# Performance work log

Hardware: AMD Instinct MI355X
Metric: run time of the kernel (lower is better)

## Reference

```python
import jax, jax.numpy as jnp
import numpy as np

# dims: L layers, T steps, N envs, D d_model, H heads, DH d_head, M mem_len, DI d_inner
L, T, N, D, H, DH, M, DI = 6, 128, 32, 1024, 16, 64, 128, 4096


def _layer_norm(x, g, b, eps=1e-5):
    mu = jnp.mean(x, axis=-1, keepdims=True)
    var = jnp.mean(jnp.square(x - mu), axis=-1, keepdims=True)
    return (x - mu) * jax.lax.rsqrt(var + eps) * g + b


def _rel_shift(x):
    # x: (n, h, q, k) with k axis indexed by relative distance (k-1 .. 0)
    n, h, q, k = x.shape
    x = jnp.pad(x, ((0, 0), (0, 0), (0, 0), (1, 0)))
    x = x.reshape(n, h, k + 1, q)[:, :, 1:, :].reshape(n, h, q, k)
    return x


def setup_inputs() -> dict:
    key = jax.random.key(0)
    ks = jax.random.split(key, 16)
    s = 0.02
    inp = {
        "x": jax.random.normal(ks[0], (T * N, D), jnp.float32),
        "context": jax.random.normal(ks[1], (T * N, D), jnp.float32),
        "mems": jax.random.normal(ks[2], (L, N, M, D), jnp.float32),
        "masks": jnp.ones((T * N,), jnp.float32),
        "Wq": jax.random.normal(ks[3], (L, D, H * DH), jnp.float32) * s,
        "Wk": jax.random.normal(ks[4], (L, D, H * DH), jnp.float32) * s,
        "Wv": jax.random.normal(ks[5], (L, D, H * DH), jnp.float32) * s,
        "Wr": jax.random.normal(ks[6], (L, D, H * DH), jnp.float32) * s,
        "Wo": jax.random.normal(ks[7], (L, H * DH, D), jnp.float32) * s,
        "W1": jax.random.normal(ks[8], (L, D, DI), jnp.float32) * s,
        "b1": jnp.zeros((L, DI), jnp.float32),
        "W2": jax.random.normal(ks[9], (L, DI, D), jnp.float32) * s,
        "b2": jnp.zeros((L, D), jnp.float32),
        "ln1_g": jnp.ones((L, D), jnp.float32),
        "ln1_b": jnp.zeros((L, D), jnp.float32),
        "ln2_g": jnp.ones((L, D), jnp.float32),
        "ln2_b": jnp.zeros((L, D), jnp.float32),
        "r_w_bias": jax.random.normal(ks[10], (H, DH), jnp.float32) * s,
        "r_r_bias": jax.random.normal(ks[11], (H, DH), jnp.float32) * s,
    }
    return inp


def reference(x, context, mems, masks, Wq, Wk, Wv, Wr, Wo, W1, b1, W2, b2,
              ln1_g, ln1_b, ln2_g, ln2_b, r_w_bias, r_r_bias):
    n = mems.shape[1]
    t = x.shape[0] // n
    m = mems.shape[2]
    klen = m + t
    dh = r_w_bias.shape[-1]
    h_heads = r_w_bias.shape[0]

    xs = x.reshape(t, n, -1)
    ctx = context.reshape(t, n, -1)
    mk = masks.reshape(t, n)

    # zero memories for envs that reset at the first step (mems * masks)
    mems = mems * mk[0][None, :, None, None]

    # episode-reset attention mask: token i attends token j iff j<=i and no
    # reset (mask==0) happened between them; memory visible only before any reset
    ep = jnp.cumsum((mk == 0.0).astype(jnp.int32), axis=0)  # (t, n)
    epT = ep.T  # (n, t)
    causal = jnp.tril(jnp.ones((t, t), bool))
    allow_seq = causal[None, :, :] & (epT[:, :, None] == epT[:, None, :])  # (n,t,t)
    allow_mem = jnp.broadcast_to((epT == 0)[:, :, None], (n, t, m))  # (n,t,m)
    allow = jnp.concatenate([allow_mem, allow_seq], axis=-1)[:, None]  # (n,1,t,K)

    # sinusoidal relative position embedding, distances klen-1 .. 0
    pos = jnp.arange(klen - 1, -1, -1, dtype=x.dtype)
    inv_freq = 1.0 / (10000.0 ** (jnp.arange(0, xs.shape[-1], 2, dtype=x.dtype) / xs.shape[-1]))
    ang = pos[:, None] * inv_freq[None, :]
    R = jnp.concatenate([jnp.sin(ang), jnp.cos(ang)], axis=-1)  # (K, D)

    h = xs + ctx  # fuse observation features with goal context
    scale = 1.0 / jnp.sqrt(jnp.asarray(dh, x.dtype))

    n_layer = mems.shape[0]
    for l in range(n_layer):
        cat = jnp.concatenate([jnp.transpose(mems[l], (1, 0, 2)), h], axis=0)  # (K,n,D)
        q = (h @ Wq[l]).reshape(t, n, h_heads, dh)
        k = (cat @ Wk[l]).reshape(klen, n, h_heads, dh)
        v = (cat @ Wv[l]).reshape(klen, n, h_heads, dh)
        r = (R @ Wr[l]).reshape(klen, h_heads, dh)
        AC = jnp.einsum('inhd,jnhd->nhij', q + r_w_bias, k)
        BD = _rel_shift(jnp.einsum('inhd,jhd->nhij', q + r_r_bias, r))
        score = (AC + BD) * scale
        score = jnp.where(allow, score, -1e9)
        attn = jax.nn.softmax(score, axis=-1)
        o = jnp.einsum('nhij,jnhd->inhd', attn, v).reshape(t, n, h_heads * dh) @ Wo[l]
        h = _layer_norm(h + o, ln1_g[l], ln1_b[l])
        f = jax.nn.relu(h @ W1[l] + b1[l]) @ W2[l] + b2[l]
        h = _layer_norm(h + f, ln2_g[l], ln2_b[l])

    return h.reshape(t * n, -1)
```

## Files before the change

kernel.cpp:

```cpp
#include <hip/hip_runtime.h>
#include <stdint.h>

#define DEV static __device__ __forceinline__

typedef __attribute__((ext_vector_type(4))) float f32x4;
typedef __attribute__((ext_vector_type(8))) short bf16x8;
typedef __attribute__((ext_vector_type(4))) short s16x4;

static constexpr int L_ = 6, T_ = 128, NE = 32, D_ = 1024, H_ = 16, DH_ = 64, M_ = 128, DI_ = 4096;
static constexpr int KLEN = M_ + T_;
static constexpr int TN = T_ * NE;
static constexpr int NB = NE * H_;

DEV unsigned short f2bf(float f) {
  unsigned u = __builtin_bit_cast(unsigned, f);
  u += 0x7FFFu + ((u >> 16) & 1u);
  return (unsigned short)(u >> 16);
}
DEV float bf2f(unsigned short h) {
  unsigned u = ((unsigned)h) << 16;
  return __builtin_bit_cast(float, u);
}

DEV void gload16(const unsigned short* g, unsigned short* lds) {
  __builtin_amdgcn_global_load_lds(
      (const __attribute__((address_space(1))) unsigned int*)g,
      (__attribute__((address_space(3))) unsigned int*)lds, 16, 0, 0);
}

#define WAITV0 asm volatile("s_waitcnt vmcnt(0)" ::: "memory")

DEV void stage128(const unsigned short* __restrict__ Ab, int lda,
                  const unsigned short* __restrict__ Bb, int ldb,
                  unsigned short* lA, unsigned short* lB,
                  int m0, int n0, int k0, int w, int l)
{
#pragma unroll
  for (int i = 0; i < 4; ++i) {
    const int obb = i * 4096 + w * 1024;
    const int ob  = obb + (l << 4);
    const int row = ob >> 7;
    const int col = (((ob >> 4) & 7) ^ (row & 7)) << 3;
    gload16(Ab + (size_t)(m0 + row) * lda + k0 + col, lA + (obb >> 1));
    gload16(Bb + (size_t)(n0 + row) * ldb + k0 + col, lB + (obb >> 1));
  }
}

DEV void compute128(const unsigned short* lA, const unsigned short* lB,
                    int w, int l, f32x4 acc[4][4])
{
  const int wr = (w >> 1) * 64, wc = (w & 1) * 64;
  const int lan = l & 15, lgr = l >> 4;
#pragma unroll
  for (int ks = 0; ks < 2; ++ks) {
    bf16x8 av[4], bv[4];
#pragma unroll
    for (int m = 0; m < 4; ++m) {
      const int row = wr + m * 16 + lan;
      const int byte = ((row << 7) + (ks << 6) + (lgr << 4)) ^ ((row & 7) << 4);
      av[m] = *(const bf16x8*)((const char*)lA + byte);
    }
#pragma unroll
    for (int n = 0; n < 4; ++n) {
      const int row = wc + n * 16 + lan;
      const int byte = ((row << 7) + (ks << 6) + (lgr << 4)) ^ ((row & 7) << 4);
      bv[n] = *(const bf16x8*)((const char*)lB + byte);
    }
#pragma unroll
    for (int m = 0; m < 4; ++m)
#pragma unroll
      for (int n = 0; n < 4; ++n)
        acc[m][n] = __builtin_amdgcn_mfma_f32_16x16x32_bf16(av[m], bv[n], acc[m][n], 0, 0, 0);
  }
}

DEV void gemm128_2ph(const unsigned short* __restrict__ Ab, int lda,
                     const unsigned short* __restrict__ Bb, int ldb,
                     unsigned short (*shA)[8192], unsigned short (*shB)[8192],
                     int m0, int n0, int nK, int w, int l, f32x4 acc[4][4])
{
  stage128(Ab, lda, Bb, ldb, shA[0], shB[0], m0, n0, 0, w, l);
  WAITV0;
  __syncthreads();
  int cur = 0;
  for (int kt = 0; kt < nK; ++kt) {
    if (kt + 1 < nK)
      stage128(Ab, lda, Bb, ldb, shA[cur ^ 1], shB[cur ^ 1], m0, n0, (kt + 1) * 64, w, l);
    compute128(shA[cur], shB[cur], w, l, acc);
    WAITV0;
    __syncthreads();
    cur ^= 1;
  }
}

template <int EPI>
__global__ __launch_bounds__(256) void gemm_bt(
    const unsigned short* __restrict__ A, int lda, int sAn, int sAh,
    const unsigned short* __restrict__ B, int ldb, int sBn, int sBh,
    void* __restrict__ Cv, int ldc, int sC,
    const float* __restrict__ bias, int nK, int Hb)
{
  __shared__ unsigned short shA[2][8192];
  __shared__ unsigned short shB[2][8192];

  const int z = blockIdx.z;
  const int bn = z / Hb, bh = z % Hb;
  const unsigned short* Ab = A + (size_t)bn * sAn + (size_t)bh * sAh;
  const unsigned short* Bb = B + (size_t)bn * sBn + (size_t)bh * sBh;
  const int m0 = blockIdx.y * 128;
  const int n0 = blockIdx.x * 128;

  const int t = threadIdx.x;
  const int w = t >> 6, l = t & 63;
  const int wr = (w >> 1) * 64, wc = (w & 1) * 64;
  const int lan = l & 15, lgr = l >> 4;

  f32x4 acc[4][4];
#pragma unroll
  for (int m = 0; m < 4; ++m)
#pragma unroll
    for (int n = 0; n < 4; ++n) acc[m][n] = (f32x4){0.f, 0.f, 0.f, 0.f};

  gemm128_2ph(Ab, lda, Bb, ldb, shA, shB, m0, n0, nK, w, l, acc);

  const int zc = z * sC;
#pragma unroll
  for (int m = 0; m < 4; ++m) {
    const int row = m0 + wr + m * 16 + lgr * 4;
#pragma unroll
    for (int n = 0; n < 4; ++n) {
      const int col = n0 + wc + n * 16 + lan;
      const float bcol = (EPI >= 2) ? bias[col] : 0.f;
#pragma unroll
      for (int e = 0; e < 4; ++e) {
        float v = acc[m][n][e];
        const size_t idx = (size_t)zc + (size_t)(row + e) * ldc + col;
        if (EPI == 0) {
          ((float*)Cv)[idx] = v;
        } else if (EPI == 1) {
          ((unsigned short*)Cv)[idx] = f2bf(v);
        } else if (EPI == 2) {
          v += bcol; v = v > 0.f ? v : 0.f;
          ((unsigned short*)Cv)[idx] = f2bf(v);
        } else {
          ((float*)Cv)[idx] = v + bcol;
        }
      }
    }
  }
}

__global__ __launch_bounds__(256) void gemm_proj(
    const unsigned short* __restrict__ catA, const unsigned short* __restrict__ wt,
    unsigned short* __restrict__ kb, unsigned short* __restrict__ vb,
    unsigned short* __restrict__ qw, unsigned short* __restrict__ qr,
    unsigned short* __restrict__ rb,
    const float* __restrict__ rwb, const float* __restrict__ rrb)
{
  __shared__ unsigned short shA[2][8192];
  __shared__ unsigned short shB[2][8192];

  const int id = blockIdx.x;
  int by, bx;
  if (id < 1024)      { by = id >> 4;               bx = id & 15; }
  else if (id < 1280) { const int u = id - 1024; by = 32 + (u >> 3); bx = 16 + (u & 7); }
  else                { const int u = id - 1280; by = 64 + (u >> 3); bx = 24 + (u & 7); }
  const int m0 = by * 128, n0 = bx * 128;

  const int t = threadIdx.x;
  const int w = t >> 6, l = t & 63;
  const int wr = (w >> 1) * 64, wc = (w & 1) * 64;
  const int lan = l & 15, lgr = l >> 4;

  f32x4 acc[4][4];
#pragma unroll
  for (int m = 0; m < 4; ++m)
#pragma unroll
    for (int n = 0; n < 4; ++n) acc[m][n] = (f32x4){0.f, 0.f, 0.f, 0.f};

  gemm128_2ph(catA, 1024, wt, 1024, shA, shB, m0, n0, 16, w, l, acc);

#pragma unroll
  for (int m = 0; m < 4; ++m) {
    const int row = m0 + wr + m * 16 + lgr * 4;
#pragma unroll
    for (int n = 0; n < 4; ++n) {
      const int col = n0 + wc + n * 16 + lan;
#pragma unroll
      for (int e = 0; e < 4; ++e) {
        const float v = acc[m][n][e];
        const int r = row + e;
        if (col < 1024) {
          kb[(size_t)r * 1024 + col] = f2bf(v);
        } else if (col < 2048) {
          vb[(size_t)r * 1024 + col - 1024] = f2bf(v);
        } else if (col < 3072) {
          const int c = col - 2048;
          const size_t o = (size_t)(r - 4096) * 1024 + c;
          qw[o] = f2bf(v + rwb[c]);
          qr[o] = f2bf(v + rrb[c]);
        } else {
          const int c = col - 3072;
          rb[(size_t)(r - 8192) * 1024 + c] = f2bf(v);
        }
      }
    }
  }
}

__global__ __launch_bounds__(256) void vtrans_kernel(
    const unsigned short* __restrict__ V, unsigned short* __restrict__ vt)
{
  __shared__ unsigned short tile[128][72];
  const int z = blockIdx.x;
  const int nn = z >> 4, hh = z & 15;
  const int t = threadIdx.x;
  for (int p = 0; p < 2; ++p) {
    const int j = p * 128 + (t >> 1);
    const int dbase = (t & 1) * 32;
    const unsigned short* src = &V[(size_t)(j * NE + nn) * 1024 + hh * 64 + dbase];
#pragma unroll
    for (int i = 0; i < 4; ++i)
      *(bf16x8*)&tile[t >> 1][dbase + i * 8] = *(const bf16x8*)&src[i * 8];
    __syncthreads();
    const int d = t >> 2, jseg = (t & 3) * 32;
    unsigned short out[32];
#pragma unroll
    for (int jj = 0; jj < 32; ++jj) out[jj] = tile[jseg + jj][d];
    unsigned short* dst = &vt[((size_t)z * 64 + d) * 256 + p * 128 + jseg];
#pragma unroll
    for (int i = 0; i < 4; ++i)
      *(bf16x8*)&dst[i * 8] = *(const bf16x8*)&out[i * 8];
    __syncthreads();
  }
}

__global__ __launch_bounds__(256) void attn_kernel(
    const unsigned short* __restrict__ qw, const unsigned short* __restrict__ qr,
    const unsigned short* __restrict__ kbf, const unsigned short* __restrict__ rbf,
    const int* __restrict__ ep, const unsigned short* __restrict__ vt,
    unsigned short* __restrict__ O)
{
  __shared__ unsigned short sS[4][32 * 256];

  const int z = blockIdx.x;
  const int nn = z >> 4, hh = z & 15;
  const int t = threadIdx.x, w = t >> 6, l = t & 63;
  const int lan = l & 15, lgr = l >> 4;
  const int i0 = w * 32;
  unsigned short* S = sS[w];

  bf16x8 av[2][2];
#pragma unroll
  for (int m = 0; m < 2; ++m)
#pragma unroll
    for (int kk = 0; kk < 2; ++kk) {
      const int i = i0 + m * 16 + lan;
      av[m][kk] = *(const bf16x8*)&qw[(size_t)(i * NE + nn) * 1024 + hh * 64 + kk * 32 + lgr * 8];
    }
#pragma unroll
  for (int n = 0; n < 16; ++n) {
    bf16x8 bv[2];
#pragma unroll
    for (int kk = 0; kk < 2; ++kk) {
      const int j = n * 16 + lan;
      bv[kk] = *(const bf16x8*)&kbf[(size_t)(j * NE + nn) * 1024 + hh * 64 + kk * 32 + lgr * 8];
    }
#pragma unroll
    for (int m = 0; m < 2; ++m) {
      f32x4 a4 = (f32x4){0.f, 0.f, 0.f, 0.f};
#pragma unroll
      for (int kk = 0; kk < 2; ++kk)
        a4 = __builtin_amdgcn_mfma_f32_16x16x32_bf16(av[m][kk], bv[kk], a4, 0, 0, 0);
#pragma unroll
      for (int e = 0; e < 4; ++e) {
        const int r = m * 16 + lgr * 4 + e;
        const int j = n * 16 + lan;
        const int swz = ((r >> 2) & 3) * 16;
        S[r * 256 + (j ^ swz)] = f2bf(a4[e]);
      }
    }
  }

  bf16x8 bq[2][2];
#pragma unroll
  for (int m = 0; m < 2; ++m)
#pragma unroll
    for (int kk = 0; kk < 2; ++kk) {
      const int i = i0 + m * 16 + lan;
      bq[m][kk] = *(const bf16x8*)&qr[(size_t)(i * NE + nn) * 1024 + hh * 64 + kk * 32 + lgr * 8];
    }
#pragma unroll
  for (int n = 0; n < 16; ++n) {
    bf16x8 bv[2];
#pragma unroll
    for (int kk = 0; kk < 2; ++kk) {
      const int jp = n * 16 + lan;
      bv[kk] = *(const bf16x8*)&rbf[(size_t)jp * 1024 + hh * 64 + kk * 32 + lgr * 8];
    }
#pragma unroll
    for (int m = 0; m < 2; ++m) {
      f32x4 a4 = (f32x4){0.f, 0.f, 0.f, 0.f};
#pragma unroll
      for (int kk = 0; kk < 2; ++kk)
        a4 = __builtin_amdgcn_mfma_f32_16x16x32_bf16(bq[m][kk], bv[kk], a4, 0, 0, 0);
#pragma unroll
      for (int e = 0; e < 4; ++e) {
        const int r = m * 16 + lgr * 4 + e;
        const int i = i0 + r;
        const int jp = n * 16 + lan;
        const int j = jp + i - 127;
        if (j >= 0 && j < 256) {
          const int swz = ((r >> 2) & 3) * 16;
          const int idx = r * 256 + (j ^ swz);
          S[idx] = f2bf(bf2f(S[idx]) + a4[e]);
        }
      }
    }
  }

  const int j0 = l * 4;
  for (int rr = 0; rr < 32; ++rr) {
    const int i = i0 + rr;
    const int epi = ep[i * NE + nn];
    const int swz = ((rr >> 2) & 3) * 16;
    s16x4 s4 = *(const s16x4*)&S[rr * 256 + (j0 ^ swz)];
    float sc[4];
#pragma unroll
    for (int q = 0; q < 4; ++q) {
      const int j = j0 + q;
      bool allow;
      if (j < M_) {
        allow = (epi == 0);
      } else {
        const int jp = j - M_;
        allow = (jp <= i) && (ep[jp * NE + nn] == epi);
      }
      sc[q] = allow ? bf2f((unsigned short)s4[q]) * 0.125f : -1e9f;
    }
    float mx = fmaxf(fmaxf(sc[0], sc[1]), fmaxf(sc[2], sc[3]));
#pragma unroll
    for (int o = 32; o; o >>= 1) mx = fmaxf(mx, __shfl_xor(mx, o));
    float p[4], sum = 0.f;
#pragma unroll
    for (int q = 0; q < 4; ++q) { p[q] = __expf(sc[q] - mx); sum += p[q]; }
#pragma unroll
    for (int o = 32; o; o >>= 1) sum += __shfl_xor(sum, o);
    const float inv = 1.f / sum;
    s16x4 o4;
#pragma unroll
    for (int q = 0; q < 4; ++q) o4[q] = (short)f2bf(p[q] * inv);
    *(s16x4*)&S[rr * 256 + (j0 ^ swz)] = o4;
  }

  const unsigned short* vtz = vt + (size_t)z * 64 * 256;
  f32x4 acc[2][4];
#pragma unroll
  for (int m = 0; m < 2; ++m)
#pragma unroll
    for (int n = 0; n < 4; ++n) acc[m][n] = (f32x4){0.f, 0.f, 0.f, 0.f};

  for (int ks = 0; ks < 8; ++ks) {
    const int kb = ks * 32 + lgr * 8;
    bf16x8 bv2[4];
#pragma unroll
    for (int n = 0; n < 4; ++n) {
      const int d = n * 16 + lan;
      bv2[n] = *(const bf16x8*)&vtz[(size_t)d * 256 + kb];
    }
    bf16x8 pa[2];
#pragma unroll
    for (int m = 0; m < 2; ++m) {
      const int r = m * 16 + lan;
      const int swz = ((r >> 2) & 3) * 16;
      pa[m] = *(const bf16x8*)&S[r * 256 + (kb ^ swz)];
    }
#pragma unroll
    for (int m = 0; m < 2; ++m)
#pragma unroll
      for (int n = 0; n < 4; ++n)
        acc[m][n] = __builtin_amdgcn_mfma_f32_16x16x32_bf16(pa[m], bv2[n], acc[m][n], 0, 0, 0);
  }
#pragma unroll
  for (int m = 0; m < 2; ++m)
#pragma unroll
    for (int n = 0; n < 4; ++n)
#pragma unroll
      for (int e = 0; e < 4; ++e) {
        const int i = i0 + m * 16 + lgr * 4 + e;
        const int d = n * 16 + lan;
        O[(size_t)(i * NE + nn) * 1024 + hh * DH_ + d] = f2bf(acc[m][n][e]);
      }
}

__global__ __launch_bounds__(256) void transpose13_kernel(
    const float* __restrict__ Wk, const float* __restrict__ Wv,
    const float* __restrict__ Wq, const float* __restrict__ Wr,
    const float* __restrict__ Wo, const float* __restrict__ W1,
    const float* __restrict__ W2,
    unsigned short* __restrict__ wtAll, unsigned short* __restrict__ wto,
    unsigned short* __restrict__ wt1, unsigned short* __restrict__ wt2)
{
  __shared__ float tile[32][33];
  const int zz = blockIdx.z;
  const float* W; unsigned short* WT; int Nd, Kd;
  if (zz < 5) {
    W = (zz == 0) ? Wk : (zz == 1) ? Wv : (zz == 2) ? Wq : (zz == 3) ? Wr : Wo;
    WT = (zz == 4) ? wto : (wtAll + (size_t)zz * 1024 * 1024);
    Nd = 1024; Kd = 1024;
  } else if (zz < 9) {
    const int c = zz - 5;
    W = W1 + (size_t)c * 1024;
    WT = wt1 + (size_t)c * 1024 * 1024;
    Nd = 4096; Kd = 1024;
  } else {
    const int c = zz - 9;
    W = W2 + (size_t)c * 1024 * 1024;
    WT = wt2 + (size_t)c * 1024;
    Nd = 1024; Kd = 4096;
  }
  const int tx = threadIdx.x & 31, ty = threadIdx.x >> 5;
  const int nIn = blockIdx.x * 32 + tx;
  const int kBase = blockIdx.y * 32;
#pragma unroll
  for (int r = 0; r < 32; r += 8)
    tile[ty + r][tx] = W[(size_t)(kBase + ty + r) * Nd + nIn];
  __syncthreads();
#pragma unroll
  for (int r = 0; r < 32; r += 8)
    WT[(size_t)(blockIdx.x * 32 + ty + r) * Kd + kBase + tx] = f2bf(tile[tx][ty + r]);
}

__global__ __launch_bounds__(256) void catmem_kernel(
    const float* __restrict__ mems_l, const float* __restrict__ masks,
    unsigned short* __restrict__ cat)
{
  const int idx = blockIdx.x * 256 + threadIdx.x;
  const int d = idx & 1023;
  const int r = idx >> 10;
  const int nn = r & 31, j = r >> 5;
  const float mk0 = masks[nn];
  cat[idx] = f2bf(mems_l[(size_t)(nn * M_ + j) * 1024 + d] * mk0);
}

__global__ __launch_bounds__(256) void hprep_kernel(
    const float* __restrict__ x, const float* __restrict__ ctx,
    float* __restrict__ h, unsigned short* __restrict__ catUp)
{
  const int idx = blockIdx.x * 256 + threadIdx.x;
  const float v = x[idx] + ctx[idx];
  h[idx] = v;
  catUp[idx] = f2bf(v);
}

__global__ __launch_bounds__(256) void rpos_kernel(unsigned short* __restrict__ R)
{
  const int idx = blockIdx.x * 256 + threadIdx.x;
  const int d = idx & 1023, j = idx >> 10;
  const float pos = (float)(KLEN - 1 - j);
  const int f = d & 511;
  const float inv_freq = __expf(-((float)(2 * f) * (1.f / 1024.f)) * 9.210340371976184f);
  const float ang = pos * inv_freq;
  const float v = (d < 512) ? sinf(ang) : cosf(ang);
  R[idx] = f2bf(v);
}

__global__ void ep_kernel(const float* __restrict__ masks, int* __restrict__ ep)
{
  const int nn = threadIdx.x;
  if (nn < NE) {
    int c = 0;
    for (int i = 0; i < T_; ++i) {
      c += (masks[i * NE + nn] == 0.f) ? 1 : 0;
      ep[i * NE + nn] = c;
    }
  }
}

template <int NP>
__global__ __launch_bounds__(256) void ln_kernel(
    const float* __restrict__ a, const float* __restrict__ parts, size_t pstride,
    const float* __restrict__ bias,
    const float* __restrict__ g, const float* __restrict__ bb,
    float* __restrict__ outf, unsigned short* __restrict__ outbf)
{
  const int row = blockIdx.x;
  const int t = threadIdx.x, w = t >> 6, l = t & 63;
  const int c = t * 4;
  const size_t base = (size_t)row * 1024;
  f32x4 v = *(const f32x4*)&a[base + c];
#pragma unroll
  for (int i = 0; i < NP; ++i)
    v = v + *(const f32x4*)&parts[i * pstride + base + c];
  if (bias) v = v + *(const f32x4*)&bias[c];
  float s = v[0] + v[1] + v[2] + v[3];
#pragma unroll
  for (int o = 32; o; o >>= 1) s += __shfl_xor(s, o);
  __shared__ float red[8];
  if (l == 0) red[w] = s;
  __syncthreads();
  s = red[0] + red[1] + red[2] + red[3];
  const float mu = s * (1.f / 1024.f);
  f32x4 dv = v - mu;
  float s2 = dv[0]*dv[0] + dv[1]*dv[1] + dv[2]*dv[2] + dv[3]*dv[3];
#pragma unroll
  for (int o = 32; o; o >>= 1) s2 += __shfl_xor(s2, o);
  if (l == 0) red[4 + w] = s2;
  __syncthreads();
  s2 = red[4] + red[5] + red[6] + red[7];
  const float inv = rsqrtf(s2 * (1.f / 1024.f) + 1e-5f);
  f32x4 y;
#pragma unroll
  for (int q = 0; q < 4; ++q) y[q] = dv[q] * inv * g[c + q] + bb[c + q];
  *(f32x4*)&outf[base + c] = y;
  if (outbf) {
    s16x4 o4;
#pragma unroll
    for (int q = 0; q < 4; ++q) o4[q] = (short)f2bf(y[q]);
    *(s16x4*)&outbf[base + c] = o4;
  }
}

extern "C" void kernel_launch(void* const* d_in, const int* in_sizes, int n_in,
                              void* d_out, int out_size, void* d_ws, size_t ws_size,
                              hipStream_t stream)
{
  (void)in_sizes; (void)n_in; (void)out_size; (void)ws_size;
  const float* x    = (const float*)d_in[0];
  const float* ctx  = (const float*)d_in[1];
  const float* mems = (const float*)d_in[2];
  const float* masks= (const float*)d_in[3];
  const float* Wq   = (const float*)d_in[4];
  const float* Wk   = (const float*)d_in[5];
  const float* Wv   = (const float*)d_in[6];
  const float* Wr   = (const float*)d_in[7];
  const float* Wo   = (const float*)d_in[8];
  const float* W1   = (const float*)d_in[9];
  const float* b1   = (const float*)d_in[10];
  const float* W2   = (const float*)d_in[11];
  const float* b2   = (const float*)d_in[12];
  const float* ln1g = (const float*)d_in[13];
  const float* ln1b = (const float*)d_in[14];
  const float* ln2g = (const float*)d_in[15];
  const float* ln2b = (const float*)d_in[16];
  const float* rwb  = (const float*)d_in[17];
  const float* rrb  = (const float*)d_in[18];

  char* ws = (char*)d_ws;
  size_t off = 0;
  auto alloc = [&](size_t bytes) {
    char* p = ws + off;
    off += (bytes + 255) & ~(size_t)255;
    return p;
  };
  unsigned short* wtAll = (unsigned short*)alloc(4096u * 1024 * 2);
  unsigned short* wto = (unsigned short*)alloc(1024u * 1024 * 2);
  unsigned short* wt1 = (unsigned short*)alloc(4096u * 1024 * 2);
  unsigned short* wt2 = (unsigned short*)alloc(4096u * 1024 * 2);
  unsigned short* cat = (unsigned short*)alloc((size_t)(KLEN * NE + 256) * 1024 * 2);
  unsigned short* rbf = (unsigned short*)alloc((size_t)KLEN * 1024 * 2);
  int*            epb = (int*)alloc((size_t)T_ * NE * 4);
  float*          h   = (float*)alloc((size_t)TN * 1024 * 4);
  float*          h1  = (float*)alloc((size_t)TN * 1024 * 4);
  unsigned short* qw  = (unsigned short*)alloc((size_t)TN * 1024 * 2);
  unsigned short* qr  = (unsigned short*)alloc((size_t)TN * 1024 * 2);
  unsigned short* kbf = (unsigned short*)alloc((size_t)KLEN * NE * 1024 * 2);
  unsigned short* vbf = (unsigned short*)alloc((size_t)KLEN * NE * 1024 * 2);
  unsigned short* vt  = (unsigned short*)alloc((size_t)NB * DH_ * KLEN * 2);
  unsigned short* ACb = (unsigned short*)alloc((size_t)NB * T_ * KLEN * 2);
  unsigned short* BDb = (unsigned short*)alloc((size_t)NB * T_ * KLEN * 2);
  unsigned short* obf = (unsigned short*)alloc((size_t)TN * 1024 * 2);

  unsigned short* catUp = cat + (size_t)M_ * NE * 1024;
  unsigned short* catR  = cat + (size_t)KLEN * NE * 1024;
  unsigned short* f1 = ACb;
  float* part = (float*)BDb;
  unsigned short* h1bf = qw;

  rpos_kernel<<<KLEN * 1024 / 256, 256, 0, stream>>>(catR);
  ep_kernel<<<1, 64, 0, stream>>>(masks, epb);
  hprep_kernel<<<TN * 1024 / 256, 256, 0, stream>>>(x, ctx, h, catUp);

  for (int l = 0; l < L_; ++l) {
    const size_t wOff = (size_t)l * 1024 * 1024;
    const size_t wOffBig = (size_t)l * 1024 * 4096;
    transpose13_kernel<<<dim3(32, 32, 13), 256, 0, stream>>>(
        Wk + wOff, Wv + wOff, Wq + wOff, Wr + wOff, Wo + wOff,
        W1 + wOffBig, W2 + wOffBig, wtAll, wto, wt1, wt2);
    catmem_kernel<<<M_ * NE * 1024 / 256, 256, 0, stream>>>(
        mems + (size_t)l * NE * M_ * 1024, masks, cat);

    gemm_proj<<<1296, 256, 0, stream>>>(cat, wtAll, kbf, vbf, qw, qr, rbf, rwb, rrb);

    vtrans_kernel<<<NB, 256, 0, stream>>>(vbf, vt);

    attn_kernel<<<NB, 256, 0, stream>>>(qw, qr, kbf, rbf, epb, vt, obf);

    gemm_bt<0><<<dim3(8, 32, 2), 256, 0, stream>>>(obf, 1024, 0, 512,
                                                   wto, 1024, 0, 512,
                                                   part, 1024, TN * 1024, nullptr, 8, 2);
    ln_kernel<2><<<TN, 256, 0, stream>>>(h, part, (size_t)TN * 1024, nullptr,
                                         ln1g + l * 1024, ln1b + l * 1024, h1, h1bf);

    gemm_bt<2><<<dim3(32, 32, 1), 256, 0, stream>>>(h1bf, 1024, 0, 0, wt1, 1024, 0, 0,
                                                    f1, 4096, 0, b1 + l * 4096, 16, 1);
    gemm_bt<0><<<dim3(8, 32, 2), 256, 0, stream>>>(f1, 4096, 0, 2048,
                                                   wt2, 4096, 0, 2048,
                                                   part, 1024, TN * 1024, nullptr, 32, 2);
    ln_kernel<2><<<TN, 256, 0, stream>>>(h1, part, (size_t)TN * 1024, b2 + l * 1024,
                                         ln2g + l * 1024, ln2b + l * 1024,
                                         (l == L_ - 1) ? (float*)d_out : h, catUp);
  }
}
```

Baseline: 1.935 ms.

## Remap GEMM blocks for XCD-aware L2 locality and drop V transpose kernel

The GEMM kernels now use a 1D grid and remap block IDs so consecutive blocks on each of the 8 XCDs cover a column strip of 8 tiles. This aims to improve L2 reuse of A and B tiles across the chiplets. Separately, the V transpose kernel is removed, and the attention kernel gathers V directly with strided scalar loads (8 per vector). That saves a launch and a round trip through memory, but the scattered 2-byte loads in the PV loop are uncoalesced and may be slow.

```diff
diff --git a/kernel.cpp b/kernel.cpp
--- a/kernel.cpp
+++ b/kernel.cpp
@@ -98,17 +98,27 @@
     const unsigned short* __restrict__ A, int lda, int sAn, int sAh,
     const unsigned short* __restrict__ B, int ldb, int sBn, int sBh,
     void* __restrict__ Cv, int ldc, int sC,
-    const float* __restrict__ bias, int nK, int Hb)
+    const float* __restrict__ bias, int nK, int Hb, int gx, int gy)
 {
   __shared__ unsigned short shA[2][8192];
   __shared__ unsigned short shB[2][8192];
 
-  const int z = blockIdx.z;
+  const int nwg = gridDim.x;
+  const int bid = blockIdx.x;
+  const int id = (bid & 7) * (nwg >> 3) + (bid >> 3);
+  const int pg = gx * gy;
+  const int z = id / pg;
+  const int rem = id - z * pg;
+  const int sc = rem / (gy * 8);
+  const int within = rem - sc * (gy * 8);
+  const int by = within >> 3;
+  const int bx = sc * 8 + (within & 7);
+
   const int bn = z / Hb, bh = z % Hb;
   const unsigned short* Ab = A + (size_t)bn * sAn + (size_t)bh * sAh;
   const unsigned short* Bb = B + (size_t)bn * sBn + (size_t)bh * sBh;
-  const int m0 = blockIdx.y * 128;
-  const int n0 = blockIdx.x * 128;
+  const int m0 = by * 128;
+  const int n0 = bx * 128;
 
   const int t = threadIdx.x;
   const int w = t >> 6, l = t & 63;
@@ -139,11 +149,9 @@
           ((float*)Cv)[idx] = v;
         } else if (EPI == 1) {
           ((unsigned short*)Cv)[idx] = f2bf(v);
-        } else if (EPI == 2) {
+        } else {
           v += bcol; v = v > 0.f ? v : 0.f;
           ((unsigned short*)Cv)[idx] = f2bf(v);
-        } else {
-          ((float*)Cv)[idx] = v + bcol;
         }
       }
     }
@@ -160,11 +168,21 @@
   __shared__ unsigned short shA[2][8192];
   __shared__ unsigned short shB[2][8192];
 
-  const int id = blockIdx.x;
+  const int bid = blockIdx.x;
+  const int id = (bid & 7) * 162 + (bid >> 3);
   int by, bx;
-  if (id < 1024)      { by = id >> 4;               bx = id & 15; }
-  else if (id < 1280) { const int u = id - 1024; by = 32 + (u >> 3); bx = 16 + (u & 7); }
-  else                { const int u = id - 1280; by = 64 + (u >> 3); bx = 24 + (u & 7); }
+  if (id < 1024) {
+    const int sc = id >> 9;
+    const int within = id & 511;
+    by = within >> 3;
+    bx = sc * 8 + (within & 7);
+  } else if (id < 1280) {
+    const int u = id - 1024;
+    by = 32 + (u >> 3); bx = 16 + (u & 7);
+  } else {
+    const int u = id - 1280;
+    by = 64 + (u >> 3); bx = 24 + (u & 7);
+  }
   const int m0 = by * 128, n0 = bx * 128;
 
   const int t = threadIdx.x;
@@ -208,37 +226,10 @@
   }
 }
 
-__global__ __launch_bounds__(256) void vtrans_kernel(
-    const unsigned short* __restrict__ V, unsigned short* __restrict__ vt)
-{
-  __shared__ unsigned short tile[128][72];
-  const int z = blockIdx.x;
-  const int nn = z >> 4, hh = z & 15;
-  const int t = threadIdx.x;
-  for (int p = 0; p < 2; ++p) {
-    const int j = p * 128 + (t >> 1);
-    const int dbase = (t & 1) * 32;
-    const unsigned short* src = &V[(size_t)(j * NE + nn) * 1024 + hh * 64 + dbase];
-#pragma unroll
-    for (int i = 0; i < 4; ++i)
-      *(bf16x8*)&tile[t >> 1][dbase + i * 8] = *(const bf16x8*)&src[i * 8];
-    __syncthreads();
-    const int d = t >> 2, jseg = (t & 3) * 32;
-    unsigned short out[32];
-#pragma unroll
-    for (int jj = 0; jj < 32; ++jj) out[jj] = tile[jseg + jj][d];
-    unsigned short* dst = &vt[((size_t)z * 64 + d) * 256 + p * 128 + jseg];
-#pragma unroll
-    for (int i = 0; i < 4; ++i)
-      *(bf16x8*)&dst[i * 8] = *(const bf16x8*)&out[i * 8];
-    __syncthreads();
-  }
-}
-
 __global__ __launch_bounds__(256) void attn_kernel(
     const unsigned short* __restrict__ qw, const unsigned short* __restrict__ qr,
     const unsigned short* __restrict__ kbf, const unsigned short* __restrict__ rbf,
-    const int* __restrict__ ep, const unsigned short* __restrict__ vt,
+    const int* __restrict__ ep, const unsigned short* __restrict__ V,
     unsigned short* __restrict__ O)
 {
   __shared__ unsigned short sS[4][32 * 256];
@@ -353,7 +344,7 @@
     *(s16x4*)&S[rr * 256 + (j0 ^ swz)] = o4;
   }
 
-  const unsigned short* vtz = vt + (size_t)z * 64 * 256;
+  const unsigned short* Vz = V + hh * DH_;
   f32x4 acc[2][4];
 #pragma unroll
   for (int m = 0; m < 2; ++m)
@@ -366,7 +357,11 @@
 #pragma unroll
     for (int n = 0; n < 4; ++n) {
       const int d = n * 16 + lan;
-      bv2[n] = *(const bf16x8*)&vtz[(size_t)d * 256 + kb];
+      bf16x8 tmp;
+#pragma unroll
+      for (int jj = 0; jj < 8; ++jj)
+        tmp[jj] = (short)Vz[(size_t)((kb + jj) * NE + nn) * 1024 + d];
+      bv2[n] = tmp;
     }
     bf16x8 pa[2];
 #pragma unroll
@@ -566,7 +561,6 @@
   unsigned short* qr  = (unsigned short*)alloc((size_t)TN * 1024 * 2);
   unsigned short* kbf = (unsigned short*)alloc((size_t)KLEN * NE * 1024 * 2);
   unsigned short* vbf = (unsigned short*)alloc((size_t)KLEN * NE * 1024 * 2);
-  unsigned short* vt  = (unsigned short*)alloc((size_t)NB * DH_ * KLEN * 2);
   unsigned short* ACb = (unsigned short*)alloc((size_t)NB * T_ * KLEN * 2);
   unsigned short* BDb = (unsigned short*)alloc((size_t)NB * T_ * KLEN * 2);
   unsigned short* obf = (unsigned short*)alloc((size_t)TN * 1024 * 2);
@@ -592,21 +586,19 @@
 
     gemm_proj<<<1296, 256, 0, stream>>>(cat, wtAll, kbf, vbf, qw, qr, rbf, rwb, rrb);
 
-    vtrans_kernel<<<NB, 256, 0, stream>>>(vbf, vt);
-
-    attn_kernel<<<NB, 256, 0, stream>>>(qw, qr, kbf, rbf, epb, vt, obf);
-
-    gemm_bt<0><<<dim3(8, 32, 2), 256, 0, stream>>>(obf, 1024, 0, 512,
-                                                   wto, 1024, 0, 512,
-                                                   part, 1024, TN * 1024, nullptr, 8, 2);
+    attn_kernel<<<NB, 256, 0, stream>>>(qw, qr, kbf, rbf, epb, vbf, obf);
+
+    gemm_bt<0><<<512, 256, 0, stream>>>(obf, 1024, 0, 512,
+                                        wto, 1024, 0, 512,
+                                        part, 1024, TN * 1024, nullptr, 8, 2, 8, 32);
     ln_kernel<2><<<TN, 256, 0, stream>>>(h, part, (size_t)TN * 1024, nullptr,
                                          ln1g + l * 1024, ln1b + l * 1024, h1, h1bf);
 
-    gemm_bt<2><<<dim3(32, 32, 1), 256, 0, stream>>>(h1bf, 1024, 0, 0, wt1, 1024, 0, 0,
-                                                    f1, 4096, 0, b1 + l * 4096, 16, 1);
-    gemm_bt<0><<<dim3(8, 32, 2), 256, 0, stream>>>(f1, 4096, 0, 2048,
-                                                   wt2, 4096, 0, 2048,
-                                                   part, 1024, TN * 1024, nullptr, 32, 2);
+    gemm_bt<2><<<1024, 256, 0, stream>>>(h1bf, 1024, 0, 0, wt1, 1024, 0, 0,
+                                         f1, 4096, 0, b1 + l * 4096, 16, 1, 32, 32);
+    gemm_bt<0><<<512, 256, 0, stream>>>(f1, 4096, 0, 2048,
+                                        wt2, 4096, 0, 2048,
+                                        part, 1024, TN * 1024, nullptr, 32, 2, 8, 32);
     ln_kernel<2><<<TN, 256, 0, stream>>>(h1, part, (size_t)TN * 1024, b2 + l * 1024,
                                          ln2g + l * 1024, ln2b + l * 1024,
                                          (l == L_ - 1) ? (float*)d_out : h, catUp);
```

Result: faster. 1.886 ms (-2.6%).
